# Optimization experiments

Measured on AMD Instinct MI355X. Metric: run time of the kernel, lower is better.

The kernel has to match this reference:

```python
import jax, jax.numpy as jnp
import numpy as np

OBS, ACT, EMB, HID, NQ = 512, 32, 512, 512, 32
B = 32768


def setup_inputs() -> dict:
    key = jax.random.key(0)
    ks = jax.random.split(key, 12)
    s_in = 1.0 / np.sqrt(OBS + ACT)
    s_emb = 1.0 / np.sqrt(EMB)
    s_hid = 1.0 / np.sqrt(HID)
    return {
        "observation": jax.random.normal(ks[0], (B, OBS), jnp.float32),
        "prev_action": jax.random.normal(ks[1], (B, ACT), jnp.float32),
        "hidden_state": jax.random.normal(ks[2], (HID,), jnp.float32),
        "cell_state": jax.random.normal(ks[3], (HID,), jnp.float32),
        "W1": jax.random.uniform(ks[4], (EMB, OBS + ACT), jnp.float32, -s_in, s_in),
        "b1": jax.random.uniform(ks[5], (EMB,), jnp.float32, -s_in, s_in),
        "W_ih": jax.random.uniform(ks[6], (4 * HID, EMB), jnp.float32, -s_hid, s_hid),
        "b_ih": jax.random.uniform(ks[7], (4 * HID,), jnp.float32, -s_hid, s_hid),
        "W_hh": jax.random.uniform(ks[8], (4 * HID, HID), jnp.float32, -s_hid, s_hid),
        "b_hh": jax.random.uniform(ks[9], (4 * HID,), jnp.float32, -s_hid, s_hid),
        "W2": jax.random.uniform(ks[10], (NQ, HID), jnp.float32, -s_hid, s_hid),
        "b2": jax.random.uniform(ks[11], (NQ,), jnp.float32, -s_hid, s_hid),
    }


def reference(observation, prev_action, hidden_state, cell_state,
              W1, b1, W_ih, b_ih, W_hh, b_hh, W2, b2):
    # MLP1: Linear + ReLU over concat(obs, prev_action)  -> [B, EMB]
    x = jnp.concatenate([observation, prev_action], axis=-1)
    x = jax.nn.relu(x @ W1.T + b1)

    # Original torch code loops LSTMCell over batch, but reuses the SAME
    # (hidden_state, cell_state) every iteration -> fully batchable.
    # gates: [B, 4H]; h contribution is identical for all rows (broadcast).
    gates = x @ W_ih.T + b_ih + (hidden_state @ W_hh.T + b_hh)
    i, f, g, o = jnp.split(gates, 4, axis=-1)  # torch LSTMCell gate order
    i = jax.nn.sigmoid(i)
    f = jax.nn.sigmoid(f)
    g = jnp.tanh(g)
    o = jax.nn.sigmoid(o)
    c_new = f * cell_state + i * g          # [B, HID]
    h_new = o * jnp.tanh(c_new)             # [B, HID]

    q_values = h_new @ W2.T + b2             # [B, NQ]
    # torch returns last loop iteration's (h, c)
    return q_values, h_new[-1], c_new[-1]
```

## Files before the change

### kernel.cpp

```cpp
#include <hip/hip_runtime.h>
#include <stdint.h>

#define DEVINL __device__ __forceinline__

typedef __attribute__((ext_vector_type(8))) __bf16 bf16x8;
typedef __attribute__((ext_vector_type(4))) float f32x4;
typedef __attribute__((ext_vector_type(16))) float f32x16;
typedef __attribute__((ext_vector_type(4))) int i32x4;
typedef __attribute__((ext_vector_type(8))) int i32x8;

DEVINL unsigned short f2bf(float f) {
  union { float f; unsigned int u; } v; v.f = f;
  unsigned int u = v.u;
  return (unsigned short)((u + 0x7fffu + ((u >> 16) & 1u)) >> 16);
}

DEVINL unsigned char f2fp8(float f) {
  return (unsigned char)(__builtin_amdgcn_cvt_pk_fp8_f32(f, f, 0, false) & 0xff);
}

DEVINL float sigm(float x) { return __builtin_amdgcn_rcpf(1.f + __expf(-x)); }
DEVINL float tanh_(float x) {
  return 1.f - 2.f * __builtin_amdgcn_rcpf(1.f + __expf(2.f * x));
}

DEVINL size_t opt_off(int row, int k) {
  return (size_t)((row >> 5) * 8 + (k >> 6)) * 2048 + ((k >> 4) & 1) * 1024 +
         ((k >> 5) & 1) * 512 + (row & 31) * 16 + (k & 15);
}

#define GLD_LDS16(gptr, lptr)                                                  \
  __builtin_amdgcn_global_load_lds(                                            \
      (__attribute__((address_space(1))) void*)(gptr),                         \
      (__attribute__((address_space(3))) void*)(lptr), 16, 0, 0)

#define TOPBAR_4 asm volatile("s_waitcnt vmcnt(4) lgkmcnt(0)\n\ts_barrier" ::: "memory")
#define TOPBAR_0 asm volatile("s_waitcnt vmcnt(0) lgkmcnt(0)\n\ts_barrier" ::: "memory")
#define BOTBAR   asm volatile("s_waitcnt lgkmcnt(0)\n\ts_barrier" ::: "memory")

DEVINL int swz_col(int c) { return ((c & 3) ^ ((c >> 3) & 3)) * 8; }

__global__ void prep_all(const float* __restrict__ obs, const float* __restrict__ act,
                         const float* __restrict__ W1, const float* __restrict__ Wih,
                         const float* __restrict__ W2, const float* __restrict__ Whh,
                         const float* __restrict__ hid, const float* __restrict__ bhh,
                         const float* __restrict__ bih,
                         unsigned short* __restrict__ A0, unsigned short* __restrict__ W1b,
                         unsigned char* __restrict__ Wih8, unsigned short* __restrict__ W2b,
                         float* __restrict__ hvec) {
  const int bid = blockIdx.x, tid = threadIdx.x;
  if (bid < 2176) {
    const int total = 32768 * 68;
    for (int c = bid * 256 + tid; c < total; c += 2176 * 256) {
      const int b = c / 68, c8 = c % 68;
      const float* src = (c8 < 64) ? (obs + (size_t)b * 512 + c8 * 8)
                                   : (act + (size_t)b * 32 + (c8 - 64) * 8);
      float4 f0 = *(const float4*)src;
      float4 f1 = *(const float4*)(src + 4);
      unsigned short u[8] = {f2bf(f0.x), f2bf(f0.y), f2bf(f0.z), f2bf(f0.w),
                             f2bf(f1.x), f2bf(f1.y), f2bf(f1.z), f2bf(f1.w)};
      *(uint4*)(A0 + (size_t)b * 544 + c8 * 8) = *(uint4*)u;
    }
  } else if (bid < 2176 + 1312) {
    const int i = (bid - 2176) * 256 + tid;
    if (i < 69632) {
      float4 f = *(const float4*)(W1 + (size_t)i * 4);
      unsigned short u[4] = {f2bf(f.x), f2bf(f.y), f2bf(f.z), f2bf(f.w)};
      *(uint2*)(W1b + (size_t)i * 4) = *(uint2*)u;
    } else if (i < 69632 + 262144) {
      const int off = i - 69632;
      const int row = off >> 7, col0 = (off & 127) * 4;
      float4 f = *(const float4*)(Wih + (size_t)off * 4);
      int pk = __builtin_amdgcn_cvt_pk_fp8_f32(f.x * 16.f, f.y * 16.f, 0, false);
      pk = __builtin_amdgcn_cvt_pk_fp8_f32(f.z * 16.f, f.w * 16.f, pk, true);
      *(unsigned int*)(Wih8 + opt_off(row, col0)) = (unsigned int)pk;
    } else {
      const int off = i - 331776;
      float4 f = *(const float4*)(W2 + (size_t)off * 4);
      unsigned short u[4] = {f2bf(f.x), f2bf(f.y), f2bf(f.z), f2bf(f.w)};
      *(uint2*)(W2b + (size_t)off * 4) = *(uint2*)u;
    }
  } else {
    const int j = (bid - 3488) * 4 + (tid >> 6);
    const int lane = tid & 63;
    const float* w = Whh + (size_t)j * 512;
    float s = 0.f;
    for (int k = lane; k < 512; k += 64) s += w[k] * hid[k];
    for (int off = 32; off; off >>= 1) s += __shfl_down(s, off, 64);
    if (lane == 0) hvec[j] = s + bhh[j] + bih[j];
  }
}

__global__ __launch_bounds__(256, 2) void gemm1_relu(
    const unsigned short* __restrict__ A0,
    const unsigned short* __restrict__ W1b,
    const float* __restrict__ b1,
    unsigned char* __restrict__ X8) {
  constexpr int KT = 17, LD = 544;
  __shared__ __align__(16) unsigned short As[2][128 * 32];
  __shared__ __align__(16) unsigned short Bs[2][128 * 32];
  const int tid = threadIdx.x, wave = tid >> 6, lane = tid & 63;
  const int id = blockIdx.x, xcd = id & 7, slot = id >> 3;
  const int m0 = (xcd * 32 + (slot >> 2)) * 128;
  const int n0 = (slot & 3) * 128;
  const int wr = (wave >> 1) * 64, wc = (wave & 1) * 64;
  f32x4 acc[4][4] = {};

  const int c0 = tid, c1 = tid + 256;
  const unsigned short* pA0 = A0 + (size_t)(m0 + (c0 >> 2)) * LD + swz_col(c0);
  const unsigned short* pA1 = A0 + (size_t)(m0 + (c1 >> 2)) * LD + swz_col(c1);
  const unsigned short* pB0 = W1b + (size_t)(n0 + (c0 >> 2)) * LD + swz_col(c0);
  const unsigned short* pB1 = W1b + (size_t)(n0 + (c1 >> 2)) * LD + swz_col(c1);
  const int fr = lane & 15, q = lane >> 4;
  const int koff = (q ^ ((fr >> 1) & 3)) * 8;

#define STAGE1(buf)                                                            \
  do {                                                                         \
    GLD_LDS16(pA0, &As[(buf)][wave * 512]);                                    \
    GLD_LDS16(pA1, &As[(buf)][2048 + wave * 512]);                             \
    GLD_LDS16(pB0, &Bs[(buf)][wave * 512]);                                    \
    GLD_LDS16(pB1, &Bs[(buf)][2048 + wave * 512]);                             \
    pA0 += 32; pA1 += 32; pB0 += 32; pB1 += 32;                                \
  } while (0)

  STAGE1(0);
  for (int kt = 0; kt < KT; ++kt) {
    if (kt + 1 < KT) { STAGE1((kt + 1) & 1); TOPBAR_4; } else { TOPBAR_0; }
    const unsigned short* as = As[kt & 1];
    const unsigned short* bs = Bs[kt & 1];
    bf16x8 a[4], b[4];
#pragma unroll
    for (int i = 0; i < 4; ++i) a[i] = *(const bf16x8*)&as[(wr + i * 16 + fr) * 32 + koff];
#pragma unroll
    for (int j = 0; j < 4; ++j) b[j] = *(const bf16x8*)&bs[(wc + j * 16 + fr) * 32 + koff];
#pragma unroll
    for (int i = 0; i < 4; ++i)
#pragma unroll
      for (int j = 0; j < 4; ++j)
        acc[i][j] = __builtin_amdgcn_mfma_f32_16x16x32_bf16(a[i], b[j], acc[i][j], 0, 0, 0);
    BOTBAR;
  }
#undef STAGE1
  const int rbase = q * 4, cn = fr;
#pragma unroll
  for (int i = 0; i < 4; ++i)
#pragma unroll
    for (int j = 0; j < 4; ++j) {
      const int gn = n0 + wc + j * 16 + cn;
      const float bias = b1[gn];
#pragma unroll
      for (int r = 0; r < 4; ++r) {
        const int gm = m0 + wr + i * 16 + rbase + r;
        float v = acc[i][j][r] + bias;
        v = v > 0.f ? v : 0.f;
        X8[opt_off(gm, gn)] = f2fp8(v * 8.f);
      }
    }
}

__global__ __launch_bounds__(256, 2) void gemm2_lstm(
    const unsigned char* __restrict__ X8,
    const unsigned char* __restrict__ Wih8,
    const float* __restrict__ hvec,
    const float* __restrict__ cell,
    unsigned short* __restrict__ H,
    float* __restrict__ hlast,
    float* __restrict__ clast) {
  __shared__ __align__(16) unsigned char Bs[4 * 16384];
  const int tid = threadIdx.x, wave = tid >> 6, lane = tid & 63;
  const int id = blockIdx.x, xcd = id & 7, slot = id >> 3;
  const int m0 = (xcd * 16 + (slot >> 4)) * 256;
  const int n0 = (slot & 15) * 32;
  const int r31 = lane & 31, g2 = lane >> 5;
  const int voff = g2 * 512 + r31 * 16;

  {
    const unsigned char* bsrc =
        Wih8 + (size_t)(wave * 16 + (n0 >> 5)) * 16384 + lane * 16;
#pragma unroll
    for (int s = 0; s < 16; ++s)
      GLD_LDS16(bsrc + s * 1024, &Bs[wave * 16384 + s * 1024]);
  }

  const unsigned char* pa = X8 + (size_t)((m0 >> 5) + wave * 2) * 16384 + voff;
  i32x8 Aa[3], Ab[3];
#define LDA(buf, kt)                                                           \
  do {                                                                         \
    i32x4 lo0 = *(const i32x4*)(pa + (kt) * 2048);                             \
    i32x4 hi0 = *(const i32x4*)(pa + (kt) * 2048 + 1024);                      \
    Aa[buf] = __builtin_shufflevector(lo0, hi0, 0, 1, 2, 3, 4, 5, 6, 7);       \
    i32x4 lo1 = *(const i32x4*)(pa + 16384 + (kt) * 2048);                     \
    i32x4 hi1 = *(const i32x4*)(pa + 16384 + (kt) * 2048 + 1024);              \
    Ab[buf] = __builtin_shufflevector(lo1, hi1, 0, 1, 2, 3, 4, 5, 6, 7);       \
  } while (0)

#define MFMA_MX(acc_, a_, b_)                                                  \
  acc_ = __builtin_amdgcn_mfma_scale_f32_32x32x64_f8f6f4(                      \
      a_, b_, acc_, 0, 0, 0, 0x7f7f7f7f, 0, 0x7f7f7f7f)

  LDA(0, 0);
  LDA(1, 1);
  __syncthreads();

  f32x16 acc00 = {}, acc01 = {}, acc02 = {}, acc03 = {};
  f32x16 acc10 = {}, acc11 = {}, acc12 = {}, acc13 = {};

#pragma unroll
  for (int kt = 0; kt < 8; ++kt) {
    const int cur = kt % 3, nx = (kt + 2) % 3;
    if (kt < 6) LDA(nx, kt + 2);
    i32x8 B0, B1, B2, B3;
    {
      const unsigned char* bb = &Bs[kt * 2048 + lane * 16];
      i32x4 l0 = *(const i32x4*)(bb);
      i32x4 h0 = *(const i32x4*)(bb + 1024);
      i32x4 l1 = *(const i32x4*)(bb + 16384);
      i32x4 h1 = *(const i32x4*)(bb + 16384 + 1024);
      i32x4 l2 = *(const i32x4*)(bb + 32768);
      i32x4 h2 = *(const i32x4*)(bb + 32768 + 1024);
      i32x4 l3 = *(const i32x4*)(bb + 49152);
      i32x4 h3 = *(const i32x4*)(bb + 49152 + 1024);
      B0 = __builtin_shufflevector(l0, h0, 0, 1, 2, 3, 4, 5, 6, 7);
      B1 = __builtin_shufflevector(l1, h1, 0, 1, 2, 3, 4, 5, 6, 7);
      B2 = __builtin_shufflevector(l2, h2, 0, 1, 2, 3, 4, 5, 6, 7);
      B3 = __builtin_shufflevector(l3, h3, 0, 1, 2, 3, 4, 5, 6, 7);
    }
    MFMA_MX(acc00, Aa[cur], B0); MFMA_MX(acc01, Aa[cur], B1);
    MFMA_MX(acc02, Aa[cur], B2); MFMA_MX(acc03, Aa[cur], B3);
    MFMA_MX(acc10, Ab[cur], B0); MFMA_MX(acc11, Ab[cur], B1);
    MFMA_MX(acc12, Ab[cur], B2); MFMA_MX(acc13, Ab[cur], B3);
  }
#undef LDA
#undef MFMA_MX

  const int gn = n0 + r31;
  const float hv_i = hvec[gn];
  const float hv_f = hvec[gn + 512];
  const float hv_g = hvec[gn + 1024];
  const float hv_o = hvec[gn + 1536];
  const float cprev = cell[gn];
  constexpr float S = 1.f / 128.f;

#define EPILOG(F, ai, af, ag, ao)                                              \
  _Pragma("unroll")                                                            \
  for (int rg = 0; rg < 4; ++rg) {                                             \
    _Pragma("unroll")                                                          \
    for (int rr = 0; rr < 4; ++rr) {                                           \
      const int reg = rg * 4 + rr;                                             \
      const int gm = m0 + wave * 64 + (F) * 32 + rr + rg * 8 + g2 * 4;         \
      float si = sigm(ai[reg] * S + hv_i);                                     \
      float sf = sigm(af[reg] * S + hv_f);                                     \
      float tg = tanh_(ag[reg] * S + hv_g);                                    \
      float so = sigm(ao[reg] * S + hv_o);                                     \
      float cnew = sf * cprev + si * tg;                                       \
      float hnew = so * tanh_(cnew);                                           \
      H[(size_t)gm * 512 + gn] = f2bf(hnew);                                   \
      if (gm == 32767) { hlast[gn] = hnew; clast[gn] = cnew; }                 \
    }                                                                          \
  }

  EPILOG(0, acc00, acc01, acc02, acc03)
  EPILOG(1, acc10, acc11, acc12, acc13)
#undef EPILOG
}

__global__ __launch_bounds__(256, 2) void gemm3(
    const unsigned short* __restrict__ H,
    const unsigned short* __restrict__ W2b,
    const float* __restrict__ b2,
    float* __restrict__ Q) {
  constexpr int LDW = 520;
  __shared__ __align__(16) unsigned short Ws[32 * LDW];
  const int tid = threadIdx.x, wave = tid >> 6, lane = tid & 63;
  const int id = blockIdx.x;
  const int m0 = ((id & 7) * 64 + (id >> 3)) * 64 + wave * 16;
  for (int c = tid; c < 2048; c += 256) {
    const int row = c >> 6, col8 = c & 63;
    *(uint4*)&Ws[row * LDW + col8 * 8] = *(const uint4*)(W2b + row * 512 + col8 * 8);
  }
  __syncthreads();

  const int fr = lane & 15, q = lane >> 4;
  f32x4 acc[2] = {};
  const unsigned short* pH = H + (size_t)(m0 + fr) * 512 + q * 8;
#pragma unroll
  for (int kt = 0; kt < 16; ++kt) {
    const int k0 = kt * 32;
    bf16x8 a  = *(const bf16x8*)(pH + k0);
    bf16x8 b0 = *(const bf16x8*)&Ws[fr * LDW + k0 + q * 8];
    bf16x8 b1 = *(const bf16x8*)&Ws[(16 + fr) * LDW + k0 + q * 8];
    acc[0] = __builtin_amdgcn_mfma_f32_16x16x32_bf16(a, b0, acc[0], 0, 0, 0);
    acc[1] = __builtin_amdgcn_mfma_f32_16x16x32_bf16(a, b1, acc[1], 0, 0, 0);
  }

  const int rbase = q * 4;
#pragma unroll
  for (int j = 0; j < 2; ++j) {
    const int gn = j * 16 + fr;
    const float bias = b2[gn];
#pragma unroll
    for (int r = 0; r < 4; ++r) {
      const int gm = m0 + rbase + r;
      Q[(size_t)gm * 32 + gn] = acc[j][r] + bias;
    }
  }
}

extern "C" void kernel_launch(void* const* d_in, const int* in_sizes, int n_in,
                              void* d_out, int out_size, void* d_ws, size_t ws_size,
                              hipStream_t stream) {
  const float* obs  = (const float*)d_in[0];
  const float* act  = (const float*)d_in[1];
  const float* hid  = (const float*)d_in[2];
  const float* cell = (const float*)d_in[3];
  const float* W1   = (const float*)d_in[4];
  const float* b1   = (const float*)d_in[5];
  const float* Wih  = (const float*)d_in[6];
  const float* bih  = (const float*)d_in[7];
  const float* Whh  = (const float*)d_in[8];
  const float* bhh  = (const float*)d_in[9];
  const float* W2   = (const float*)d_in[10];
  const float* b2   = (const float*)d_in[11];
  float* out = (float*)d_out;

  char* ws = (char*)d_ws;
  unsigned short* A0   = (unsigned short*)(ws);
  unsigned short* H    = (unsigned short*)(ws);
  unsigned char*  X8   = (unsigned char*)(ws + 35651584);
  unsigned short* W1b  = (unsigned short*)(ws + 52428800);
  unsigned char*  Wih8 = (unsigned char*)(ws + 52985856);
  unsigned short* W2b  = (unsigned short*)(ws + 54034432);
  float*          hvec = (float*)(ws + 54067200);

  prep_all<<<4000, 256, 0, stream>>>(obs, act, W1, Wih, W2, Whh, hid, bhh, bih,
                                     A0, W1b, Wih8, W2b, hvec);
  gemm1_relu<<<1024, 256, 0, stream>>>(A0, W1b, b1, X8);
  gemm2_lstm<<<2048, 256, 0, stream>>>(X8, Wih8, hvec, cell, H,
                                       out + 32768 * 32,
                                       out + 32768 * 32 + 512);
  gemm3<<<512, 256, 0, stream>>>(H, W2b, b2, out);
}
```

Baseline: 208.1 us.

## Fuse fp32-to-bf16 activation conversion into gemm1 A-tile loading

Removes the separate pass in prep_all that converted observation and prev_action to a bf16 A0 buffer. gemm1 now loads fp32 activations straight into registers, converts them with v_cvt_pk_bf16_f32, and writes the swizzled bf16 tile to LDS, while W1 is still loaded with direct global-to-LDS transfers. This avoids writing and re-reading about 35 MB of intermediate data. In exchange, gemm1 reads twice as many bytes for A, and each k-step now waits for all outstanding loads (vmcnt(0)) with a single barrier, which reduces overlap between loads and MFMA work.

```diff
diff --git a/kernel.cpp b/kernel.cpp
--- a/kernel.cpp
+++ b/kernel.cpp
@@ -15,6 +15,12 @@
   return (unsigned short)((u + 0x7fffu + ((u >> 16) & 1u)) >> 16);
 }
 
+DEVINL unsigned int cvtpk_bf16(float lo, float hi) {
+  unsigned int r;
+  asm("v_cvt_pk_bf16_f32 %0, %1, %2" : "=v"(r) : "v"(lo), "v"(hi));
+  return r;
+}
+
 DEVINL unsigned char f2fp8(float f) {
   return (unsigned char)(__builtin_amdgcn_cvt_pk_fp8_f32(f, f, 0, false) & 0xff);
 }
@@ -34,35 +40,20 @@
       (__attribute__((address_space(1))) void*)(gptr),                         \
       (__attribute__((address_space(3))) void*)(lptr), 16, 0, 0)
 
-#define TOPBAR_4 asm volatile("s_waitcnt vmcnt(4) lgkmcnt(0)\n\ts_barrier" ::: "memory")
-#define TOPBAR_0 asm volatile("s_waitcnt vmcnt(0) lgkmcnt(0)\n\ts_barrier" ::: "memory")
-#define BOTBAR   asm volatile("s_waitcnt lgkmcnt(0)\n\ts_barrier" ::: "memory")
+#define KT_BAR asm volatile("s_waitcnt vmcnt(0) lgkmcnt(0)\n\ts_barrier" ::: "memory")
 
 DEVINL int swz_col(int c) { return ((c & 3) ^ ((c >> 3) & 3)) * 8; }
 
-__global__ void prep_all(const float* __restrict__ obs, const float* __restrict__ act,
-                         const float* __restrict__ W1, const float* __restrict__ Wih,
+__global__ void prep_all(const float* __restrict__ W1, const float* __restrict__ Wih,
                          const float* __restrict__ W2, const float* __restrict__ Whh,
                          const float* __restrict__ hid, const float* __restrict__ bhh,
                          const float* __restrict__ bih,
-                         unsigned short* __restrict__ A0, unsigned short* __restrict__ W1b,
+                         unsigned short* __restrict__ W1b,
                          unsigned char* __restrict__ Wih8, unsigned short* __restrict__ W2b,
                          float* __restrict__ hvec) {
   const int bid = blockIdx.x, tid = threadIdx.x;
-  if (bid < 2176) {
-    const int total = 32768 * 68;
-    for (int c = bid * 256 + tid; c < total; c += 2176 * 256) {
-      const int b = c / 68, c8 = c % 68;
-      const float* src = (c8 < 64) ? (obs + (size_t)b * 512 + c8 * 8)
-                                   : (act + (size_t)b * 32 + (c8 - 64) * 8);
-      float4 f0 = *(const float4*)src;
-      float4 f1 = *(const float4*)(src + 4);
-      unsigned short u[8] = {f2bf(f0.x), f2bf(f0.y), f2bf(f0.z), f2bf(f0.w),
-                             f2bf(f1.x), f2bf(f1.y), f2bf(f1.z), f2bf(f1.w)};
-      *(uint4*)(A0 + (size_t)b * 544 + c8 * 8) = *(uint4*)u;
-    }
-  } else if (bid < 2176 + 1312) {
-    const int i = (bid - 2176) * 256 + tid;
+  if (bid < 1312) {
+    const int i = bid * 256 + tid;
     if (i < 69632) {
       float4 f = *(const float4*)(W1 + (size_t)i * 4);
       unsigned short u[4] = {f2bf(f.x), f2bf(f.y), f2bf(f.z), f2bf(f.w)};
@@ -81,7 +72,7 @@
       *(uint2*)(W2b + (size_t)off * 4) = *(uint2*)u;
     }
   } else {
-    const int j = (bid - 3488) * 4 + (tid >> 6);
+    const int j = (bid - 1312) * 4 + (tid >> 6);
     const int lane = tid & 63;
     const float* w = Whh + (size_t)j * 512;
     float s = 0.f;
@@ -92,13 +83,14 @@
 }
 
 __global__ __launch_bounds__(256, 2) void gemm1_relu(
-    const unsigned short* __restrict__ A0,
+    const float* __restrict__ obs,
+    const float* __restrict__ act,
     const unsigned short* __restrict__ W1b,
     const float* __restrict__ b1,
     unsigned char* __restrict__ X8) {
-  constexpr int KT = 17, LD = 544;
-  __shared__ __align__(16) unsigned short As[2][128 * 32];
-  __shared__ __align__(16) unsigned short Bs[2][128 * 32];
+  constexpr int KT = 17;
+  __shared__ __align__(16) unsigned short As[2][4096];
+  __shared__ __align__(16) unsigned short Bs[2][4096];
   const int tid = threadIdx.x, wave = tid >> 6, lane = tid & 63;
   const int id = blockIdx.x, xcd = id & 7, slot = id >> 3;
   const int m0 = (xcd * 32 + (slot >> 2)) * 128;
@@ -107,25 +99,52 @@
   f32x4 acc[4][4] = {};
 
   const int c0 = tid, c1 = tid + 256;
-  const unsigned short* pA0 = A0 + (size_t)(m0 + (c0 >> 2)) * LD + swz_col(c0);
-  const unsigned short* pA1 = A0 + (size_t)(m0 + (c1 >> 2)) * LD + swz_col(c1);
-  const unsigned short* pB0 = W1b + (size_t)(n0 + (c0 >> 2)) * LD + swz_col(c0);
-  const unsigned short* pB1 = W1b + (size_t)(n0 + (c1 >> 2)) * LD + swz_col(c1);
+  const int r0 = c0 >> 2, r1 = c1 >> 2;
+  const int sw0 = swz_col(c0), sw1 = swz_col(c1);
+  const float* pObs0 = obs + (size_t)(m0 + r0) * 512 + sw0;
+  const float* pObs1 = obs + (size_t)(m0 + r1) * 512 + sw1;
+  const float* pAct0 = act + (size_t)(m0 + r0) * 32 + sw0;
+  const float* pAct1 = act + (size_t)(m0 + r1) * 32 + sw1;
+  const unsigned short* pB0 = W1b + (size_t)(n0 + r0) * 544 + sw0;
+  const unsigned short* pB1 = W1b + (size_t)(n0 + r1) * 544 + sw1;
   const int fr = lane & 15, q = lane >> 4;
   const int koff = (q ^ ((fr >> 1) & 3)) * 8;
 
-#define STAGE1(buf)                                                            \
+  float4 fA00, fA01, fA10, fA11;
+
+#define LOADA(kt)                                                              \
   do {                                                                         \
-    GLD_LDS16(pA0, &As[(buf)][wave * 512]);                                    \
-    GLD_LDS16(pA1, &As[(buf)][2048 + wave * 512]);                             \
+    const float* s0_ = ((kt) < 16) ? (pObs0 + (kt) * 32) : pAct0;              \
+    const float* s1_ = ((kt) < 16) ? (pObs1 + (kt) * 32) : pAct1;              \
+    fA00 = *(const float4*)s0_; fA01 = *(const float4*)(s0_ + 4);              \
+    fA10 = *(const float4*)s1_; fA11 = *(const float4*)(s1_ + 4);              \
+  } while (0)
+
+#define GLDB(buf)                                                              \
+  do {                                                                         \
     GLD_LDS16(pB0, &Bs[(buf)][wave * 512]);                                    \
     GLD_LDS16(pB1, &Bs[(buf)][2048 + wave * 512]);                             \
-    pA0 += 32; pA1 += 32; pB0 += 32; pB1 += 32;                                \
+    pB0 += 32; pB1 += 32;                                                      \
   } while (0)
 
-  STAGE1(0);
+#define CVTWR(buf)                                                             \
+  do {                                                                         \
+    unsigned int w0_[4] = {cvtpk_bf16(fA00.x, fA00.y), cvtpk_bf16(fA00.z, fA00.w), \
+                           cvtpk_bf16(fA01.x, fA01.y), cvtpk_bf16(fA01.z, fA01.w)}; \
+    *(uint4*)&As[(buf)][c0 * 8] = *(uint4*)w0_;                                \
+    unsigned int w1_[4] = {cvtpk_bf16(fA10.x, fA10.y), cvtpk_bf16(fA10.z, fA10.w), \
+                           cvtpk_bf16(fA11.x, fA11.y), cvtpk_bf16(fA11.z, fA11.w)}; \
+    *(uint4*)&As[(buf)][c1 * 8] = *(uint4*)w1_;                                \
+  } while (0)
+
+  LOADA(0);
+  GLDB(0);
+  CVTWR(0);
+  KT_BAR;
+
+#pragma unroll
   for (int kt = 0; kt < KT; ++kt) {
-    if (kt + 1 < KT) { STAGE1((kt + 1) & 1); TOPBAR_4; } else { TOPBAR_0; }
+    if (kt < 16) { LOADA(kt + 1); GLDB((kt + 1) & 1); }
     const unsigned short* as = As[kt & 1];
     const unsigned short* bs = Bs[kt & 1];
     bf16x8 a[4], b[4];
@@ -138,9 +157,15 @@
 #pragma unroll
       for (int j = 0; j < 4; ++j)
         acc[i][j] = __builtin_amdgcn_mfma_f32_16x16x32_bf16(a[i], b[j], acc[i][j], 0, 0, 0);
-    BOTBAR;
-  }
-#undef STAGE1
+    if (kt < 16) {
+      CVTWR((kt + 1) & 1);
+      KT_BAR;
+    }
+  }
+#undef LOADA
+#undef GLDB
+#undef CVTWR
+
   const int rbase = q * 4, cn = fr;
 #pragma unroll
   for (int i = 0; i < 4; ++i)
@@ -324,7 +349,6 @@
   float* out = (float*)d_out;
 
   char* ws = (char*)d_ws;
-  unsigned short* A0   = (unsigned short*)(ws);
   unsigned short* H    = (unsigned short*)(ws);
   unsigned char*  X8   = (unsigned char*)(ws + 35651584);
   unsigned short* W1b  = (unsigned short*)(ws + 52428800);
@@ -332,9 +356,9 @@
   unsigned short* W2b  = (unsigned short*)(ws + 54034432);
   float*          hvec = (float*)(ws + 54067200);
 
-  prep_all<<<4000, 256, 0, stream>>>(obs, act, W1, Wih, W2, Whh, hid, bhh, bih,
-                                     A0, W1b, Wih8, W2b, hvec);
-  gemm1_relu<<<1024, 256, 0, stream>>>(A0, W1b, b1, X8);
+  prep_all<<<1824, 256, 0, stream>>>(W1, Wih, W2, Whh, hid, bhh, bih,
+                                     W1b, Wih8, W2b, hvec);
+  gemm1_relu<<<1024, 256, 0, stream>>>(obs, act, W1b, b1, X8);
   gemm2_lstm<<<2048, 256, 0, stream>>>(X8, Wih8, hvec, cell, H,
                                        out + 32768 * 32,
                                        out + 32768 * 32 + 512);
```

New measurement: 219.7 us. +5.6%, slower.
